# Kernel tuning notes

Measured on AMD Instinct MI355X. Metric: run time of the kernel, lower is better.

## Reference

```python
import jax, jax.numpy as jnp
import numpy as np

B, NB, T, C, H = 4, 256, 33, 512, 8
HD = C // H
SCALE = HD ** -0.5


def setup_inputs() -> dict:
    key = jax.random.key(0)
    ks = jax.random.split(key, 8)
    x = jax.random.normal(ks[0], (B, NB * T, C), jnp.float32)
    m = jax.random.randint(ks[1], (NB, T, T), 0, 2)
    eye = jnp.eye(T, dtype=m.dtype)
    attn_mask = jnp.maximum(m, eye[None, :, :]).astype(jnp.int32)  # diag always attendable
    edge_feats = jax.random.normal(ks[2], (NB, T, T, 4), jnp.float32)
    Wqkv = jax.random.normal(ks[3], (3 * C, C), jnp.float32) * (C ** -0.5)
    bqkv = jnp.zeros((3 * C,), jnp.float32)
    Wproj = jax.random.normal(ks[4], (C, C), jnp.float32) * (C ** -0.5)
    bproj = jnp.zeros((C,), jnp.float32)
    Wgate = jax.random.normal(ks[5], (H, 4), jnp.float32) * 0.01  # init.normal_(std=0.01)
    bgate = jnp.zeros((H,), jnp.float32)
    return dict(x=x, attn_mask=attn_mask, edge_feats=edge_feats,
                Wqkv=Wqkv, bqkv=bqkv, Wproj=Wproj, bproj=bproj,
                Wgate=Wgate, bgate=bgate)


def reference(x, attn_mask, edge_feats, Wqkv, bqkv, Wproj, bproj, Wgate, bgate):
    Bq, N, Cd = x.shape
    x_blk = x.reshape(Bq, NB, T, Cd)                         # (B,nb,T,C)
    qkv = x_blk @ Wqkv.T + bqkv                              # (B,nb,T,3C)
    q, k, v = jnp.split(qkv, 3, axis=-1)
    q = q.reshape(Bq, NB, T, H, HD)
    k = k.reshape(Bq, NB, T, H, HD)
    v = v.reshape(Bq, NB, T, H, HD)
    scores = jnp.einsum('bnqhd,bnkhd->bnqkh', q, k) * SCALE  # (B,nb,T,T,H)

    # physics bias: copy edge_feats[...,:4], overwrite diagonal to (0,0,0,1)
    bias = jnp.broadcast_to(edge_feats[None, ..., :4], (Bq, NB, T, T, 4))
    eye = jnp.eye(T, dtype=bool)[None, None, :, :, None]
    diag_vals = jnp.array([0.0, 0.0, 0.0, 1.0], dtype=bias.dtype)
    bias = jnp.where(eye, diag_vals, bias)

    scores = scores + bias[..., 3:4]                         # broadcast over heads
    mask_e = (attn_mask[None, :, :, :, None] != 0)           # (1,nb,T,T,1)
    scores = jnp.where(mask_e, scores, -jnp.inf)
    probs = jax.nn.softmax(scores, axis=3)                   # softmax over keys

    gates = bias @ Wgate.T + bgate                           # (B,nb,T,T,H)
    gates = jnp.where(mask_e, gates, 0.0)
    cw = probs + gates                                       # combined weights

    out = jnp.einsum('bnqkh,bnkhd->bnqhd', cw, v).reshape(Bq, NB, T, Cd)
    out = out @ Wproj.T + bproj
    return out.reshape(Bq, NB * T, Cd)
```

## Files before the change

kernel.cpp:

```cpp
#include <hip/hip_runtime.h>

typedef _Float16 half8 __attribute__((ext_vector_type(8)));
typedef _Float16 half4v __attribute__((ext_vector_type(4)));
typedef float floatx4 __attribute__((ext_vector_type(4)));
typedef unsigned uint4v __attribute__((ext_vector_type(4)));
typedef unsigned uint2v __attribute__((ext_vector_type(2)));

#define KDIM 512

__device__ __forceinline__ void gll16(const _Float16* g, void* l) {
  __builtin_amdgcn_global_load_lds((const __attribute__((address_space(1))) void*)g,
                                   (__attribute__((address_space(3))) void*)l, 16, 0, 0);
}

__device__ __forceinline__ unsigned pack2(float a, float b) {
  return __builtin_bit_cast(unsigned, __builtin_amdgcn_cvt_pkrtz(a, b));
}

__global__ void cvt_all(const float* __restrict__ x, const float* __restrict__ wq,
                        const float* __restrict__ wp, _Float16* __restrict__ xh,
                        _Float16* __restrict__ wqh, _Float16* __restrict__ wph) {
  long stride = (long)gridDim.x * blockDim.x;
  long t0 = (long)blockIdx.x * blockDim.x + threadIdx.x;
  for (long i = t0; i < 17301504L/4; i += stride) {
    float4 v = ((const float4*)x)[i];
    half4v h; h[0]=(_Float16)v.x; h[1]=(_Float16)v.y; h[2]=(_Float16)v.z; h[3]=(_Float16)v.w;
    ((half4v*)xh)[i] = h;
  }
  for (long i = t0; i < 786432L/4; i += stride) {
    float4 v = ((const float4*)wq)[i];
    half4v h; h[0]=(_Float16)v.x; h[1]=(_Float16)v.y; h[2]=(_Float16)v.z; h[3]=(_Float16)v.w;
    ((half4v*)wqh)[i] = h;
  }
  for (long i = t0; i < 262144L/4; i += stride) {
    float4 v = ((const float4*)wp)[i];
    half4v h; h[0]=(_Float16)v.x; h[1]=(_Float16)v.y; h[2]=(_Float16)v.z; h[3]=(_Float16)v.w;
    ((half4v*)wph)[i] = h;
  }
}

template<int NN, bool OUTF16>
__global__ __launch_bounds__(256, 2) void gemm_bt(const _Float16* __restrict__ A,
    const _Float16* __restrict__ Bw, const float* __restrict__ bias,
    void* __restrict__ Cout) {
  __shared__ __attribute__((aligned(16))) _Float16 As[128*64];
  __shared__ __attribute__((aligned(16))) _Float16 Bs[128*64];
  const int ntile = NN / 128;
  int bid = blockIdx.x;
  int mt = bid / ntile, nt = bid % ntile;
  int tid = threadIdx.x;
  int lane = tid & 63;
  int w = tid >> 6, wr = w >> 1, wc = w & 1;
  int g = lane >> 4, c = lane & 15;
  long arow0 = (long)mt * 128;
  int bcol0 = nt * 128;
  floatx4 acc[4][4];
#pragma unroll
  for (int i = 0; i < 4; i++)
#pragma unroll
    for (int j = 0; j < 4; j++) acc[i][j] = (floatx4)0.0f;

  int wbase = tid & ~63;
  for (int kt = 0; kt < KDIM / 64; ++kt) {
    if (kt) __syncthreads();
    int k0 = kt * 64;
#pragma unroll
    for (int j = 0; j < 4; ++j) {
      int idx = j * 256 + tid;
      int row = idx >> 3;
      int sc = (idx & 7) ^ (row & 7);
      gll16(A + ((arow0 + row) * KDIM + k0 + sc * 8), (char*)As + (j * 256 + wbase) * 16);
      gll16(Bw + ((long)(bcol0 + row) * KDIM + k0 + sc * 8), (char*)Bs + (j * 256 + wbase) * 16);
    }
    __syncthreads();
#pragma unroll
    for (int ks = 0; ks < 2; ++ks) {
      half8 af[4], bf[4];
      int cb = ks * 64 + g * 16;
#pragma unroll
      for (int i = 0; i < 4; ++i) {
        int ra = wr * 64 + i * 16 + c;
        af[i] = *(const half8*)((const char*)As + ra * 128 + (cb ^ ((ra & 7) << 4)));
        int rb = wc * 64 + i * 16 + c;
        bf[i] = *(const half8*)((const char*)Bs + rb * 128 + (cb ^ ((rb & 7) << 4)));
      }
#pragma unroll
      for (int mi = 0; mi < 4; mi++)
#pragma unroll
        for (int ni = 0; ni < 4; ni++)
          acc[mi][ni] = __builtin_amdgcn_mfma_f32_16x16x32_f16(af[mi], bf[ni], acc[mi][ni], 0, 0, 0);
    }
  }
  long crow0 = arow0 + wr * 64;
  int ccol0 = bcol0 + wc * 64;
#pragma unroll
  for (int mi = 0; mi < 4; mi++) {
#pragma unroll
    for (int ni = 0; ni < 4; ni++) {
      int col = ccol0 + ni * 16 + c;
      float bv = bias[col];
#pragma unroll
      for (int j = 0; j < 4; j++) {
        long r = crow0 + mi * 16 + g * 4 + j;
        float v = acc[mi][ni][j] + bv;
        if (OUTF16) ((_Float16*)Cout)[r * NN + col] = (_Float16)v;
        else        ((float*)Cout)[r * NN + col] = v;
      }
    }
  }
}

__global__ __launch_bounds__(256, 4) void attn_mid(const _Float16* __restrict__ qkv,
    const int* __restrict__ amask, const float* __restrict__ ef,
    const float* __restrict__ Wg, const float* __restrict__ bg,
    _Float16* __restrict__ aout) {
  __shared__ __attribute__((aligned(16))) half4v efT[48][42];
  __shared__ __attribute__((aligned(16))) _Float16 outb[4][33][88];
  __shared__ unsigned long long mrow[48];
  int blk = blockIdx.x;
  int nb = blk & 255;
  long R0 = (long)blk * 33;
  int tid = threadIdx.x;
  int lane = tid & 63, w = tid >> 6;
  int g = lane >> 4, c = lane & 15;

  if (tid < 48) {
    unsigned long long bits = 0;
    if (tid < 33) {
      const int* mp = amask + ((long)nb * 33 + tid) * 33;
      for (int k = 0; k < 33; k++) if (mp[k]) bits |= (1ull << k);
    }
    mrow[tid] = bits;
  }
  for (int u = tid; u < 48 * 42; u += 256) {
    int k = u / 42, q = u - k * 42;
    half4v hv; hv[0] = (_Float16)0.f; hv[1] = (_Float16)0.f; hv[2] = (_Float16)0.f; hv[3] = (_Float16)0.f;
    if (q < 33 && k < 33) {
      if (q == k) hv[3] = (_Float16)1.0f;
      else {
        float4 e4 = *(const float4*)(ef + (((long)nb * 33 + q) * 33 + k) * 4);
        hv[0] = (_Float16)e4.x; hv[1] = (_Float16)e4.y; hv[2] = (_Float16)e4.z; hv[3] = (_Float16)e4.w;
      }
    }
    efT[k][q] = hv;
  }
  __syncthreads();

  for (int hh = 0; hh < 2; ++hh) {
    int h = w + 4 * hh;
    float wg0 = Wg[h * 4 + 0], wg1 = Wg[h * 4 + 1], wg2 = Wg[h * 4 + 2], wg3 = Wg[h * 4 + 3];
    float bgh = bg[h];
    half8 qf[3][2], kf[3][2];
#pragma unroll
    for (int t3 = 0; t3 < 3; ++t3) {
      int t = t3 * 16 + c;
      long tr = R0 + (t < 33 ? t : 0);
#pragma unroll
      for (int ks = 0; ks < 2; ++ks) {
        int d0 = ks * 32 + g * 8;
        qf[t3][ks] = *(const half8*)(qkv + tr * 1536 + h * 64 + d0);
        kf[t3][ks] = *(const half8*)(qkv + tr * 1536 + 512 + h * 64 + d0);
      }
    }
    floatx4 s[3][3];
#pragma unroll
    for (int kt = 0; kt < 3; kt++)
#pragma unroll
      for (int qt = 0; qt < 3; qt++) s[kt][qt] = (floatx4)0.0f;
#pragma unroll
    for (int ks = 0; ks < 2; ++ks)
#pragma unroll
      for (int kt = 0; kt < 3; kt++)
#pragma unroll
        for (int qt = 0; qt < 3; qt++)
          s[kt][qt] = __builtin_amdgcn_mfma_f32_16x16x32_f16(kf[kt][ks], qf[qt][ks], s[kt][qt], 0, 0, 0);

    unsigned pk[2][3][2];
    float cw32[3];
#pragma unroll
    for (int qt = 0; qt < 3; qt++) {
      int q = qt * 16 + c;
      unsigned long long mb = mrow[q];
      float sv[3][4];
#pragma unroll
      for (int kt = 0; kt < 3; kt++)
#pragma unroll
        for (int j = 0; j < 4; j++) {
          int k = kt * 16 + 4 * g + j;
          float e3 = (float)efT[k][q][3];
          bool mk = (mb >> k) & 1;
          sv[kt][j] = mk ? s[kt][qt][j] * 0.125f + e3 : -1e30f;
        }
      float m = sv[0][0];
#pragma unroll
      for (int kt = 0; kt < 3; kt++)
#pragma unroll
        for (int j = 0; j < 4; j++) m = fmaxf(m, sv[kt][j]);
      m = fmaxf(m, __shfl_xor(m, 16, 64));
      m = fmaxf(m, __shfl_xor(m, 32, 64));
      float p[3][4], sum = 0.f;
#pragma unroll
      for (int kt = 0; kt < 3; kt++)
#pragma unroll
        for (int j = 0; j < 4; j++) { p[kt][j] = __expf(sv[kt][j] - m); sum += p[kt][j]; }
      sum += __shfl_xor(sum, 16, 64);
      sum += __shfl_xor(sum, 32, 64);
      float inv = __builtin_amdgcn_rcpf(sum);
      float cw[3][4];
#pragma unroll
      for (int kt = 0; kt < 3; kt++)
#pragma unroll
        for (int j = 0; j < 4; j++) {
          int k = kt * 16 + 4 * g + j;
          bool mk = (mb >> k) & 1;
          half4v e = efT[k][q];
          float gate = (float)e[0] * wg0 + (float)e[1] * wg1 + (float)e[2] * wg2 + (float)e[3] * wg3 + bgh;
          cw[kt][j] = mk ? p[kt][j] * inv + gate : 0.0f;
        }
#pragma unroll
      for (int kt = 0; kt < 2; kt++)
#pragma unroll
        for (int jp = 0; jp < 2; jp++) pk[kt][qt][jp] = pack2(cw[kt][2 * jp], cw[kt][2 * jp + 1]);
      cw32[qt] = cw[2][0];
    }

    half8 pb[3];
#pragma unroll
    for (int qt = 0; qt < 3; qt++) {
      uint4v d;
#pragma unroll
      for (int w2 = 0; w2 < 4; w2++) {
        int srcl = (((g & 1) * 2 + (w2 >> 1)) << 4) | c;
        unsigned v0 = (unsigned)__shfl((int)pk[0][qt][w2 & 1], srcl, 64);
        unsigned v1 = (unsigned)__shfl((int)pk[1][qt][w2 & 1], srcl, 64);
        d[w2] = (g >> 1) ? v1 : v0;
      }
      pb[qt] = __builtin_bit_cast(half8, d);
    }

    floatx4 o[4][3];
#pragma unroll
    for (int dt = 0; dt < 4; dt++)
#pragma unroll
      for (int qt = 0; qt < 3; qt++) o[dt][qt] = (floatx4)0.0f;
#pragma unroll
    for (int dh = 0; dh < 2; dh++) {
      half8 vf[2];
#pragma unroll
      for (int di = 0; di < 2; di++) {
        int dt = dh * 2 + di;
        half8 v;
#pragma unroll
        for (int e = 0; e < 8; e++)
          v[e] = qkv[(R0 + g * 8 + e) * 1536 + 1024 + h * 64 + dt * 16 + c];
        vf[di] = v;
      }
#pragma unroll
      for (int di = 0; di < 2; di++)
#pragma unroll
        for (int qt = 0; qt < 3; qt++)
          o[dh * 2 + di][qt] = __builtin_amdgcn_mfma_f32_16x16x32_f16(vf[di], pb[qt], o[dh * 2 + di][qt], 0, 0, 0);
    }
    float p32[3];
#pragma unroll
    for (int qt = 0; qt < 3; qt++) p32[qt] = __shfl(cw32[qt], c, 64);
#pragma unroll
    for (int dt = 0; dt < 4; dt++) {
      half4v v32 = *(const half4v*)(qkv + (R0 + 32) * 1536 + 1024 + h * 64 + dt * 16 + 4 * g);
#pragma unroll
      for (int qt = 0; qt < 3; qt++)
#pragma unroll
        for (int j = 0; j < 4; j++) o[dt][qt][j] += (float)v32[j] * p32[qt];
    }

#pragma unroll
    for (int qt = 0; qt < 3; qt++) {
      int q = qt * 16 + c;
      if (q < 33) {
#pragma unroll
        for (int dt = 0; dt < 4; dt++) {
          uint2v uu;
          uu[0] = pack2(o[dt][qt][0], o[dt][qt][1]);
          uu[1] = pack2(o[dt][qt][2], o[dt][qt][3]);
          *(uint2v*)&outb[w][q][dt * 16 + 4 * g] = uu;
        }
      }
    }
#pragma unroll
    for (int r0 = 0; r0 < 5; ++r0) {
      int q = r0 * 8 + (lane >> 3);
      if (q < 33) {
        half8 vv = *(const half8*)&outb[w][q][(lane & 7) * 8];
        *(half8*)(aout + (R0 + q) * 512 + h * 64 + (lane & 7) * 8) = vv;
      }
    }
  }
}

extern "C" void kernel_launch(void* const* d_in, const int* in_sizes, int n_in,
                              void* d_out, int out_size, void* d_ws, size_t ws_size,
                              hipStream_t stream) {
  const float* x  = (const float*)d_in[0];
  const int*   am = (const int*)d_in[1];
  const float* ef = (const float*)d_in[2];
  const float* Wq = (const float*)d_in[3];
  const float* bq = (const float*)d_in[4];
  const float* Wp = (const float*)d_in[5];
  const float* bp = (const float*)d_in[6];
  const float* Wg = (const float*)d_in[7];
  const float* bg = (const float*)d_in[8];
  char* ws = (char*)d_ws;
  _Float16* xh   = (_Float16*)(ws);
  _Float16* wqh  = (_Float16*)(ws + 34603008L);
  _Float16* wph  = (_Float16*)(ws + 36175872L);
  _Float16* qkv  = (_Float16*)(ws + 36700160L);
  _Float16* aout = (_Float16*)(ws + 140509184L);

  hipLaunchKernelGGL(cvt_all, dim3(2048), dim3(256), 0, stream, x, Wq, Wp, xh, wqh, wph);
  hipLaunchKernelGGL((gemm_bt<1536, true>), dim3(264 * 12), dim3(256), 0, stream, xh, wqh, bq, (void*)qkv);
  hipLaunchKernelGGL(attn_mid, dim3(1024), dim3(256), 0, stream, qkv, am, ef, Wg, bg, aout);
  hipLaunchKernelGGL((gemm_bt<512, false>), dim3(264 * 4), dim3(256), 0, stream, aout, wph, bp, (float*)d_out);
}
```

Before: 155.1 us.

## Replace QKV GEMM with 256x256 double-buffered tile kernel and XCD-aware block remap

Adds a new gemm256 kernel for the QKV projection. It uses 256x256 output tiles with 8 waves, double-buffered LDS staging through global_load_lds, MFMA priority boosts, and a block-index remap that groups tiles per XCD. The larger tiles are meant to raise operand reuse and cut global traffic, and the prefetch of two k-steps ahead aims to overlap loads with MFMA. In exchange it uses 128KB of LDS per block, which limits occupancy, and it launches fewer workgroups (792).

```diff
diff --git a/kernel.cpp b/kernel.cpp
--- a/kernel.cpp
+++ b/kernel.cpp
@@ -37,6 +37,130 @@
     half4v h; h[0]=(_Float16)v.x; h[1]=(_Float16)v.y; h[2]=(_Float16)v.z; h[3]=(_Float16)v.w;
     ((half4v*)wph)[i] = h;
   }
+}
+
+__global__ __launch_bounds__(512, 2) void gemm256(const _Float16* __restrict__ A,
+    const _Float16* __restrict__ Bw, const float* __restrict__ bias,
+    _Float16* __restrict__ Cout) {
+  __shared__ __attribute__((aligned(16))) _Float16 As[2][256 * 64];
+  __shared__ __attribute__((aligned(16))) _Float16 Bs[2][256 * 64];
+  const int NN = 1536, ntile = NN / 256;
+  int nwg = gridDim.x;
+  int q8 = nwg >> 3;
+  int bid = blockIdx.x;
+  int wg = (bid & 7) * q8 + (bid >> 3);
+  int mt = wg / ntile, nt = wg % ntile;
+  long arow0 = (long)mt * 256;
+  int bcol0 = nt * 256;
+  int tid = threadIdx.x;
+  int lane = tid & 63, w = tid >> 6;
+  int wr = w >> 2, wc = w & 3;
+  int g = lane >> 4, c = lane & 15;
+
+  auto STAGE = [&](int b, int kt) {
+    int k0 = kt * 64;
+#pragma unroll
+    for (int u = 0; u < 4; ++u) {
+      int L = u * 512 + tid;
+      int row = L >> 3, sl = (L & 7) ^ (row & 7);
+      char* da = (char*)&As[b][0] + u * 8192 + (tid & ~63) * 16;
+      char* db = (char*)&Bs[b][0] + u * 8192 + (tid & ~63) * 16;
+      gll16(A + (arow0 + row) * KDIM + k0 + sl * 8, da);
+      gll16(Bw + (long)(bcol0 + row) * KDIM + k0 + sl * 8, db);
+    }
+  };
+
+  floatx4 acc[8][4];
+#pragma unroll
+  for (int i = 0; i < 8; i++)
+#pragma unroll
+    for (int j = 0; j < 4; j++) acc[i][j] = (floatx4)0.0f;
+
+  STAGE(0, 0);
+  STAGE(1, 1);
+  asm volatile("s_waitcnt vmcnt(8)" ::: "memory");
+  __builtin_amdgcn_sched_barrier(0);
+  __builtin_amdgcn_s_barrier();
+
+  for (int kt = 0; kt < 8; ++kt) {
+    int cur = kt & 1;
+    half8 bf[4][2];
+#pragma unroll
+    for (int nf = 0; nf < 4; ++nf) {
+      int rb = wc * 64 + nf * 16 + c;
+      const char* base = (const char*)&Bs[cur][0] + rb * 128;
+      int x7 = (rb & 7) << 4;
+#pragma unroll
+      for (int ks = 0; ks < 2; ++ks)
+        bf[nf][ks] = *(const half8*)(base + ((ks * 64 + g * 16) ^ x7));
+    }
+    half8 af[4][2];
+#pragma unroll
+    for (int i = 0; i < 4; ++i) {
+      int ra = wr * 128 + i * 16 + c;
+      const char* base = (const char*)&As[cur][0] + ra * 128;
+      int x7 = (ra & 7) << 4;
+#pragma unroll
+      for (int ks = 0; ks < 2; ++ks)
+        af[i][ks] = *(const half8*)(base + ((ks * 64 + g * 16) ^ x7));
+    }
+    __builtin_amdgcn_s_setprio(1);
+#pragma unroll
+    for (int ks = 0; ks < 2; ++ks)
+#pragma unroll
+      for (int i = 0; i < 4; ++i)
+#pragma unroll
+        for (int nf = 0; nf < 4; ++nf)
+          acc[i][nf] = __builtin_amdgcn_mfma_f32_16x16x32_f16(af[i][ks], bf[nf][ks], acc[i][nf], 0, 0, 0);
+    __builtin_amdgcn_s_setprio(0);
+    __builtin_amdgcn_sched_barrier(0);
+#pragma unroll
+    for (int i = 0; i < 4; ++i) {
+      int ra = wr * 128 + 64 + i * 16 + c;
+      const char* base = (const char*)&As[cur][0] + ra * 128;
+      int x7 = (ra & 7) << 4;
+#pragma unroll
+      for (int ks = 0; ks < 2; ++ks)
+        af[i][ks] = *(const half8*)(base + ((ks * 64 + g * 16) ^ x7));
+    }
+    asm volatile("s_waitcnt lgkmcnt(0)" ::: "memory");
+    __builtin_amdgcn_sched_barrier(0);
+    __builtin_amdgcn_s_barrier();
+    if (kt + 2 < 8) STAGE(cur, kt + 2);
+    __builtin_amdgcn_s_setprio(1);
+#pragma unroll
+    for (int ks = 0; ks < 2; ++ks)
+#pragma unroll
+      for (int i = 0; i < 4; ++i)
+#pragma unroll
+        for (int nf = 0; nf < 4; ++nf)
+          acc[4 + i][nf] = __builtin_amdgcn_mfma_f32_16x16x32_f16(af[i][ks], bf[nf][ks], acc[4 + i][nf], 0, 0, 0);
+    __builtin_amdgcn_s_setprio(0);
+    if (kt < 7) {
+      if (kt + 2 < 8) {
+        asm volatile("s_waitcnt vmcnt(8)" ::: "memory");
+      } else {
+        asm volatile("s_waitcnt vmcnt(0)" ::: "memory");
+      }
+      __builtin_amdgcn_sched_barrier(0);
+      __builtin_amdgcn_s_barrier();
+    }
+  }
+
+  long crow0 = arow0 + wr * 128;
+  int ccol0 = bcol0 + wc * 64;
+#pragma unroll
+  for (int mi = 0; mi < 8; mi++)
+#pragma unroll
+    for (int ni = 0; ni < 4; ni++) {
+      int col = ccol0 + ni * 16 + c;
+      float bv = bias[col];
+#pragma unroll
+      for (int j = 0; j < 4; j++) {
+        long r = crow0 + mi * 16 + g * 4 + j;
+        Cout[r * NN + col] = (_Float16)(acc[mi][ni][j] + bv);
+      }
+    }
 }
 
 template<int NN, bool OUTF16>
@@ -317,7 +441,7 @@
   _Float16* aout = (_Float16*)(ws + 140509184L);
 
   hipLaunchKernelGGL(cvt_all, dim3(2048), dim3(256), 0, stream, x, Wq, Wp, xh, wqh, wph);
-  hipLaunchKernelGGL((gemm_bt<1536, true>), dim3(264 * 12), dim3(256), 0, stream, xh, wqh, bq, (void*)qkv);
+  hipLaunchKernelGGL(gemm256, dim3(132 * 6), dim3(512), 0, stream, xh, wqh, bq, qkv);
   hipLaunchKernelGGL(attn_mid, dim3(1024), dim3(256), 0, stream, qkv, am, ef, Wg, bg, aout);
   hipLaunchKernelGGL((gemm_bt<512, false>), dim3(264 * 4), dim3(256), 0, stream, aout, wph, bp, (float*)d_out);
 }
```

New measurement: 156.4 us. About the same (+0.9%).

## Replace GEMM with 256x256-tile, 8-wave, double-buffered pipelined kernel

Applied to the files above, without the earlier changes.

Rewrites both GEMMs to use 256x256 output tiles with 512-thread blocks (8 waves). K is split into half-steps that are double-buffered in LDS, so the next tile's global loads run while MFMAs consume the current one, gated by explicit vmcnt waits and s_setprio. Block IDs are remapped across 8 groups, likely to spread tiles across XCDs for L2 locality. The larger tiles cut redundant global loads, but there are fewer workgroups (264 for the projection GEMM) and register pressure is higher with 32 accumulators per wave.

```diff
diff --git a/kernel.cpp b/kernel.cpp
--- a/kernel.cpp
+++ b/kernel.cpp
@@ -40,61 +40,119 @@
 }
 
 template<int NN, bool OUTF16>
-__global__ __launch_bounds__(256, 2) void gemm_bt(const _Float16* __restrict__ A,
+__global__ __launch_bounds__(512, 2) void gemm8p(const _Float16* __restrict__ A,
     const _Float16* __restrict__ Bw, const float* __restrict__ bias,
     void* __restrict__ Cout) {
-  __shared__ __attribute__((aligned(16))) _Float16 As[128*64];
-  __shared__ __attribute__((aligned(16))) _Float16 Bs[128*64];
-  const int ntile = NN / 128;
+  __shared__ __attribute__((aligned(16))) _Float16 SH[2][2][2][8192];
+  const int ntile = NN / 256;
+  int nwg = gridDim.x;
+  int q8 = nwg >> 3;
   int bid = blockIdx.x;
-  int mt = bid / ntile, nt = bid % ntile;
+  int wg = (bid & 7) * q8 + (bid >> 3);
+  int mt = wg / ntile, nt = wg % ntile;
+  long arow0 = (long)mt * 256;
+  int bcol0 = nt * 256;
   int tid = threadIdx.x;
-  int lane = tid & 63;
-  int w = tid >> 6, wr = w >> 1, wc = w & 1;
+  int lane = tid & 63, w = tid >> 6;
+  int wr = w >> 2, wc = w & 3;
   int g = lane >> 4, c = lane & 15;
-  long arow0 = (long)mt * 128;
-  int bcol0 = nt * 128;
-  floatx4 acc[4][4];
-#pragma unroll
-  for (int i = 0; i < 4; i++)
+
+  auto STAGE = [&](int b, int m, int h, int kt) {
+    int k0 = kt * 64 + h * 32;
+    const _Float16* src = m ? Bw : A;
+    long r0 = m ? (long)bcol0 : arow0;
+#pragma unroll
+    for (int r = 0; r < 2; ++r) {
+      int L = r * 512 + tid;
+      int row = L >> 2;
+      int sl = (L & 3) ^ ((row >> 1) & 3);
+      char* dst = (char*)&SH[b][m][h][0] + r * 8192 + (tid & ~63) * 16;
+      gll16(src + (r0 + row) * KDIM + k0 + sl * 8, dst);
+    }
+  };
+  auto AFRAG = [&](int b, int h, int mi) -> half8 {
+    int ra = wr * 128 + mi * 16 + c;
+    return *(const half8*)((const char*)&SH[b][0][h][0] + ra * 64 +
+                           ((g * 16) ^ (((ra >> 1) & 3) << 4)));
+  };
+  auto BFRAG = [&](int b, int h, int ni) -> half8 {
+    int rb = wc * 64 + ni * 16 + c;
+    return *(const half8*)((const char*)&SH[b][1][h][0] + rb * 64 +
+                           ((g * 16) ^ (((rb >> 1) & 3) << 4)));
+  };
+
+  floatx4 acc[8][4];
+#pragma unroll
+  for (int i = 0; i < 8; i++)
 #pragma unroll
     for (int j = 0; j < 4; j++) acc[i][j] = (floatx4)0.0f;
 
-  int wbase = tid & ~63;
-  for (int kt = 0; kt < KDIM / 64; ++kt) {
-    if (kt) __syncthreads();
-    int k0 = kt * 64;
-#pragma unroll
-    for (int j = 0; j < 4; ++j) {
-      int idx = j * 256 + tid;
-      int row = idx >> 3;
-      int sc = (idx & 7) ^ (row & 7);
-      gll16(A + ((arow0 + row) * KDIM + k0 + sc * 8), (char*)As + (j * 256 + wbase) * 16);
-      gll16(Bw + ((long)(bcol0 + row) * KDIM + k0 + sc * 8), (char*)Bs + (j * 256 + wbase) * 16);
-    }
-    __syncthreads();
-#pragma unroll
-    for (int ks = 0; ks < 2; ++ks) {
-      half8 af[4], bf[4];
-      int cb = ks * 64 + g * 16;
-#pragma unroll
-      for (int i = 0; i < 4; ++i) {
-        int ra = wr * 64 + i * 16 + c;
-        af[i] = *(const half8*)((const char*)As + ra * 128 + (cb ^ ((ra & 7) << 4)));
-        int rb = wc * 64 + i * 16 + c;
-        bf[i] = *(const half8*)((const char*)Bs + rb * 128 + (cb ^ ((rb & 7) << 4)));
-      }
-#pragma unroll
-      for (int mi = 0; mi < 4; mi++)
-#pragma unroll
-        for (int ni = 0; ni < 4; ni++)
-          acc[mi][ni] = __builtin_amdgcn_mfma_f32_16x16x32_f16(af[mi], bf[ni], acc[mi][ni], 0, 0, 0);
-    }
-  }
-  long crow0 = arow0 + wr * 64;
+  STAGE(0, 0, 0, 0); STAGE(0, 1, 0, 0); STAGE(0, 0, 1, 0); STAGE(0, 1, 1, 0);
+
+  half8 a0[8], a1[8], b0[4], b1[4];
+  for (int kt = 0; kt < 8; ++kt) {
+    int cur = kt & 1, nxt = cur ^ 1;
+    bool st = kt < 7;
+    asm volatile("s_waitcnt vmcnt(4)" ::: "memory");
+    __builtin_amdgcn_sched_barrier(0);
+    __builtin_amdgcn_s_barrier();
+    if (st) STAGE(nxt, 0, 0, kt + 1);
+#pragma unroll
+    for (int mi = 0; mi < 8; ++mi) a0[mi] = AFRAG(cur, 0, mi);
+#pragma unroll
+    for (int ni = 0; ni < 2; ++ni) b0[ni] = BFRAG(cur, 0, ni);
+    __builtin_amdgcn_s_setprio(1);
+#pragma unroll
+    for (int mi = 0; mi < 8; ++mi)
+#pragma unroll
+      for (int ni = 0; ni < 2; ++ni)
+        acc[mi][ni] = __builtin_amdgcn_mfma_f32_16x16x32_f16(a0[mi], b0[ni], acc[mi][ni], 0, 0, 0);
+    __builtin_amdgcn_s_setprio(0);
+    if (st) STAGE(nxt, 1, 0, kt + 1);
+#pragma unroll
+    for (int ni = 2; ni < 4; ++ni) b0[ni] = BFRAG(cur, 0, ni);
+    __builtin_amdgcn_s_setprio(1);
+#pragma unroll
+    for (int mi = 0; mi < 8; ++mi)
+#pragma unroll
+      for (int ni = 2; ni < 4; ++ni)
+        acc[mi][ni] = __builtin_amdgcn_mfma_f32_16x16x32_f16(a0[mi], b0[ni], acc[mi][ni], 0, 0, 0);
+    __builtin_amdgcn_s_setprio(0);
+    if (kt < 7) {
+      asm volatile("s_waitcnt vmcnt(4)" ::: "memory");
+    } else {
+      asm volatile("s_waitcnt vmcnt(0)" ::: "memory");
+    }
+    __builtin_amdgcn_sched_barrier(0);
+    __builtin_amdgcn_s_barrier();
+    if (st) STAGE(nxt, 0, 1, kt + 1);
+#pragma unroll
+    for (int mi = 0; mi < 8; ++mi) a1[mi] = AFRAG(cur, 1, mi);
+#pragma unroll
+    for (int ni = 0; ni < 2; ++ni) b1[ni] = BFRAG(cur, 1, ni);
+    __builtin_amdgcn_s_setprio(1);
+#pragma unroll
+    for (int mi = 0; mi < 8; ++mi)
+#pragma unroll
+      for (int ni = 0; ni < 2; ++ni)
+        acc[mi][ni] = __builtin_amdgcn_mfma_f32_16x16x32_f16(a1[mi], b1[ni], acc[mi][ni], 0, 0, 0);
+    __builtin_amdgcn_s_setprio(0);
+    if (st) STAGE(nxt, 1, 1, kt + 1);
+#pragma unroll
+    for (int ni = 2; ni < 4; ++ni) b1[ni] = BFRAG(cur, 1, ni);
+    __builtin_amdgcn_s_setprio(1);
+#pragma unroll
+    for (int mi = 0; mi < 8; ++mi)
+#pragma unroll
+      for (int ni = 2; ni < 4; ++ni)
+        acc[mi][ni] = __builtin_amdgcn_mfma_f32_16x16x32_f16(a1[mi], b1[ni], acc[mi][ni], 0, 0, 0);
+    __builtin_amdgcn_s_setprio(0);
+  }
+
+  long crow0 = arow0 + wr * 128;
   int ccol0 = bcol0 + wc * 64;
 #pragma unroll
-  for (int mi = 0; mi < 4; mi++) {
+  for (int mi = 0; mi < 8; mi++)
 #pragma unroll
     for (int ni = 0; ni < 4; ni++) {
       int col = ccol0 + ni * 16 + c;
@@ -107,7 +165,6 @@
         else        ((float*)Cout)[r * NN + col] = v;
       }
     }
-  }
 }
 
 __global__ __launch_bounds__(256, 4) void attn_mid(const _Float16* __restrict__ qkv,
@@ -317,7 +374,7 @@
   _Float16* aout = (_Float16*)(ws + 140509184L);
 
   hipLaunchKernelGGL(cvt_all, dim3(2048), dim3(256), 0, stream, x, Wq, Wp, xh, wqh, wph);
-  hipLaunchKernelGGL((gemm_bt<1536, true>), dim3(264 * 12), dim3(256), 0, stream, xh, wqh, bq, (void*)qkv);
+  hipLaunchKernelGGL((gemm8p<1536, true>), dim3(792), dim3(512), 0, stream, xh, wqh, bq, (void*)qkv);
   hipLaunchKernelGGL(attn_mid, dim3(1024), dim3(256), 0, stream, qkv, am, ef, Wg, bg, aout);
-  hipLaunchKernelGGL((gemm_bt<512, false>), dim3(264 * 4), dim3(256), 0, stream, aout, wph, bp, (float*)d_out);
-}
+  hipLaunchKernelGGL((gemm8p<512, false>), dim3(264), dim3(512), 0, stream, aout, wph, bp, (void*)d_out);
+}
```

Measured after the change: 163.8 us. +5.6%, slower.

## Double-buffer A tile in LDS, read weights directly from global, remap blocks

Applied to the files above, without the earlier changes.

Rewrites the projection GEMM kernel to double-buffer only the activation tile in LDS, issuing async global-to-LDS loads two K-steps ahead with explicit waitcnt and barrier control. Weight fragments are now read straight from global memory, which is meant to rely on L2 hits instead of staging them in LDS. The block index is remapped so that blocks on the same XCD-style stride group share M tiles and iterate N tiles outward. MFMA runs at raised wave priority and occupancy is raised to 3 blocks per CU. Uncached global weight loads could add latency, and the hand-written vmcnt counts have to match the number of loads issued per stage.

```diff
diff --git a/kernel.cpp b/kernel.cpp
--- a/kernel.cpp
+++ b/kernel.cpp
@@ -40,57 +40,92 @@
 }
 
 template<int NN, bool OUTF16>
-__global__ __launch_bounds__(256, 2) void gemm_bt(const _Float16* __restrict__ A,
+__global__ __launch_bounds__(256, 3) void gemm_bl2(const _Float16* __restrict__ A,
     const _Float16* __restrict__ Bw, const float* __restrict__ bias,
     void* __restrict__ Cout) {
-  __shared__ __attribute__((aligned(16))) _Float16 As[128*64];
-  __shared__ __attribute__((aligned(16))) _Float16 Bs[128*64];
+  __shared__ __attribute__((aligned(16))) _Float16 As[2][128 * 64];
   const int ntile = NN / 128;
+  int nwg = gridDim.x;
+  int q8 = nwg >> 3;
   int bid = blockIdx.x;
-  int mt = bid / ntile, nt = bid % ntile;
-  int tid = threadIdx.x;
-  int lane = tid & 63;
-  int w = tid >> 6, wr = w >> 1, wc = w & 1;
-  int g = lane >> 4, c = lane & 15;
+  int wg = (bid & 7) * q8 + (bid >> 3);
+  int mt = wg % 264, nt = wg / 264;
   long arow0 = (long)mt * 128;
   int bcol0 = nt * 128;
-  floatx4 acc[4][4];
-#pragma unroll
-  for (int i = 0; i < 4; i++)
-#pragma unroll
-    for (int j = 0; j < 4; j++) acc[i][j] = (floatx4)0.0f;
-
+  int tid = threadIdx.x;
+  int lane = tid & 63, w = tid >> 6;
+  int wr = w >> 1, wc = w & 1;
+  int g = lane >> 4, c = lane & 15;
   int wbase = tid & ~63;
-  for (int kt = 0; kt < KDIM / 64; ++kt) {
-    if (kt) __syncthreads();
+
+  auto STAGE = [&](int b, int kt) {
     int k0 = kt * 64;
 #pragma unroll
     for (int j = 0; j < 4; ++j) {
       int idx = j * 256 + tid;
       int row = idx >> 3;
-      int sc = (idx & 7) ^ (row & 7);
-      gll16(A + ((arow0 + row) * KDIM + k0 + sc * 8), (char*)As + (j * 256 + wbase) * 16);
-      gll16(Bw + ((long)(bcol0 + row) * KDIM + k0 + sc * 8), (char*)Bs + (j * 256 + wbase) * 16);
-    }
-    __syncthreads();
-#pragma unroll
-    for (int ks = 0; ks < 2; ++ks) {
-      half8 af[4], bf[4];
-      int cb = ks * 64 + g * 16;
-#pragma unroll
-      for (int i = 0; i < 4; ++i) {
-        int ra = wr * 64 + i * 16 + c;
-        af[i] = *(const half8*)((const char*)As + ra * 128 + (cb ^ ((ra & 7) << 4)));
-        int rb = wc * 64 + i * 16 + c;
-        bf[i] = *(const half8*)((const char*)Bs + rb * 128 + (cb ^ ((rb & 7) << 4)));
-      }
-#pragma unroll
-      for (int mi = 0; mi < 4; mi++)
-#pragma unroll
-        for (int ni = 0; ni < 4; ni++)
-          acc[mi][ni] = __builtin_amdgcn_mfma_f32_16x16x32_f16(af[mi], bf[ni], acc[mi][ni], 0, 0, 0);
-    }
-  }
+      int sl = (idx & 7) ^ (row & 7);
+      gll16(A + ((arow0 + row) * KDIM + k0 + sl * 8),
+            (char*)&As[b][0] + (j * 256 + wbase) * 16);
+    }
+  };
+
+  floatx4 acc[4][4];
+#pragma unroll
+  for (int i = 0; i < 4; i++)
+#pragma unroll
+    for (int j = 0; j < 4; j++) acc[i][j] = (floatx4)0.0f;
+
+  STAGE(0, 0);
+  STAGE(1, 1);
+  asm volatile("s_waitcnt vmcnt(4)" ::: "memory");
+  __builtin_amdgcn_sched_barrier(0);
+  __builtin_amdgcn_s_barrier();
+
+  for (int kt = 0; kt < 8; ++kt) {
+    int cur = kt & 1;
+    half8 bf[4][2];
+#pragma unroll
+    for (int ni = 0; ni < 4; ++ni) {
+      long brow = bcol0 + wc * 64 + ni * 16 + c;
+#pragma unroll
+      for (int ks = 0; ks < 2; ++ks)
+        bf[ni][ks] = *(const half8*)(Bw + brow * KDIM + kt * 64 + ks * 32 + g * 8);
+    }
+    half8 af[4][2];
+#pragma unroll
+    for (int mi = 0; mi < 4; ++mi) {
+      int ra = wr * 64 + mi * 16 + c;
+      const char* base = (const char*)&As[cur][0] + ra * 128;
+      int x7 = (ra & 7) << 4;
+#pragma unroll
+      for (int ks = 0; ks < 2; ++ks)
+        af[mi][ks] = *(const half8*)(base + ((ks * 64 + g * 16) ^ x7));
+    }
+    asm volatile("s_waitcnt lgkmcnt(0)" ::: "memory");
+    __builtin_amdgcn_sched_barrier(0);
+    __builtin_amdgcn_s_barrier();
+    if (kt + 2 < 8) STAGE(cur, kt + 2);
+    __builtin_amdgcn_s_setprio(1);
+#pragma unroll
+    for (int ks = 0; ks < 2; ++ks)
+#pragma unroll
+      for (int mi = 0; mi < 4; ++mi)
+#pragma unroll
+        for (int ni = 0; ni < 4; ++ni)
+          acc[mi][ni] = __builtin_amdgcn_mfma_f32_16x16x32_f16(af[mi][ks], bf[ni][ks], acc[mi][ni], 0, 0, 0);
+    __builtin_amdgcn_s_setprio(0);
+    if (kt < 7) {
+      if (kt + 2 < 8) {
+        asm volatile("s_waitcnt vmcnt(4)" ::: "memory");
+      } else {
+        asm volatile("s_waitcnt vmcnt(0)" ::: "memory");
+      }
+      __builtin_amdgcn_sched_barrier(0);
+      __builtin_amdgcn_s_barrier();
+    }
+  }
+
   long crow0 = arow0 + wr * 64;
   int ccol0 = bcol0 + wc * 64;
 #pragma unroll
@@ -317,7 +352,7 @@
   _Float16* aout = (_Float16*)(ws + 140509184L);
 
   hipLaunchKernelGGL(cvt_all, dim3(2048), dim3(256), 0, stream, x, Wq, Wp, xh, wqh, wph);
-  hipLaunchKernelGGL((gemm_bt<1536, true>), dim3(264 * 12), dim3(256), 0, stream, xh, wqh, bq, (void*)qkv);
+  hipLaunchKernelGGL((gemm_bl2<1536, true>), dim3(264 * 12), dim3(256), 0, stream, xh, wqh, bq, (void*)qkv);
   hipLaunchKernelGGL(attn_mid, dim3(1024), dim3(256), 0, stream, qkv, am, ef, Wg, bg, aout);
-  hipLaunchKernelGGL((gemm_bt<512, false>), dim3(264 * 4), dim3(256), 0, stream, aout, wph, bp, (float*)d_out);
-}
+  hipLaunchKernelGGL((gemm_bl2<512, false>), dim3(264 * 4), dim3(256), 0, stream, aout, wph, bp, (void*)d_out);
+}
```

After: 235.8 us. +52.1%, slower.
